# Kernel tuning notes

Hardware: AMD Instinct MI355X
Metric: run time of the kernel (lower is better)

Reference implementation:

```python
import jax, jax.numpy as jnp
import numpy as np

IN_CH = 128
OUT_CH = 128
INPUT_LEN = 512
KERNEL = 8
STRIDE = 1
OUT_LEN = (INPUT_LEN - KERNEL) // STRIDE + 1  # 505
BATCH = 64


def setup_inputs() -> dict:
    key = jax.random.key(0)
    kx, kw, kb = jax.random.split(key, 3)
    x = jax.random.normal(kx, (BATCH, IN_CH, INPUT_LEN), dtype=jnp.float32)
    weight = jax.random.normal(kw, (OUT_LEN, OUT_CH, IN_CH, KERNEL), dtype=jnp.float32)
    bias = jax.random.normal(kb, (OUT_CH, OUT_LEN), dtype=jnp.float32)
    return {"x": x, "weight": weight, "bias": bias}


def reference(x, weight, bias):
    # unfold: gather sliding windows -> [b, i, l_out, k]
    idx = jnp.arange(OUT_LEN)[:, None] * STRIDE + jnp.arange(KERNEL)[None, :]  # [l, k]
    x_unf = x[:, :, idx]  # [b, i, l, k]
    # per-position independent GEMM: 'blik,loik->bol' with x permuted to bilk
    out = jnp.einsum('bilk,loik->bol', x_unf, weight)
    out = out + bias[None, :, :]
    return out
```

## Files before the change

### kernel.cpp

```cpp
#include <hip/hip_runtime.h>
#include <hip/hip_bf16.h>

#define BATCH 64
#define IN_CH 128
#define ILEN  512
#define OLEN  505
#define OCH   128
#define KDIM  1024
#define BK    64
#define NCHK  16
#define NWG   (OLEN * 2)

typedef float f32x4  __attribute__((ext_vector_type(4)));
typedef short bf16x8 __attribute__((ext_vector_type(8)));

__device__ __forceinline__ short f2bf(float f) {
  union { __hip_bfloat16 h; short s; } u;
  u.h = __float2bfloat16(f);
  return u.s;
}

template <bool USE_TMP>
__global__ __launch_bounds__(256, 2) void lc1d_main(
    const float* __restrict__ x, const float* __restrict__ w,
    const float* __restrict__ bias, float* __restrict__ outp) {
  const int orig = blockIdx.x;
  const int xcd = orig & 7, idx = orig >> 3;
  const int q = NWG / 8, rm = NWG % 8;
  const int wg = (xcd < rm ? xcd * (q + 1) : rm * (q + 1) + (xcd - rm) * q) + idx;
  const int l  = wg >> 1;
  const int oh = wg & 1;

  const int tid  = threadIdx.x;
  const int lane = tid & 63;
  const int wn   = tid >> 6;
  const int r    = lane & 15;
  const int h    = lane >> 4;

  __shared__ float Bs[3][BK * 64];
  __shared__ short As[2][BK * 64];

  f32x4 acc[4];
#pragma unroll
  for (int m = 0; m < 4; ++m) acc[m] = (f32x4){0.f, 0.f, 0.f, 0.f};

  const float* __restrict__ wl =
      w + (size_t)l * (OCH * KDIM) + (size_t)oh * 64 * KDIM;

  const int so  = tid >> 4;
  const int sc  = tid & 15;
  const int ssw = ((so & 7) << 1) | ((so >> 3) & 1);

  const int kk  = tid & 63;
  const int tb  = tid >> 6;
  const int il  = kk >> 3;
  const int kof = kk & 7;

  float aa0[16], aa1[16];

  auto loadA = [&](float (&aa)[16], int kc) {
    const float* xb = x + (size_t)(kc * 8 + il) * ILEN + l + kof;
#pragma unroll
    for (int it = 0; it < 16; ++it)
      aa[it] = xb[(size_t)(it * 4 + tb) * (IN_CH * ILEN)];
  };
  auto writeA = [&](const float (&aa)[16], int buf) {
#pragma unroll
    for (int it = 0; it < 16; ++it) {
      const int b = it * 4 + tb;
      As[buf][b * 64 + (kk ^ ((b & 7) << 3))] = f2bf(aa[it]);
    }
  };
  auto stageB = [&](int buf, int kc) {
#pragma unroll
    for (int it = 0; it < 4; ++it) {
      const int ob = it * 16 + so;
      const float* src = wl + (size_t)ob * KDIM + kc * BK + (sc ^ ssw) * 4;
      __builtin_amdgcn_global_load_lds(
          (const __attribute__((address_space(1))) void*)src,
          (__attribute__((address_space(3))) void*)&Bs[buf][ob * 64 + sc * 4],
          16, 0, 0);
    }
  };

  const int rsw = ((r & 7) << 1) | ((r >> 3) & 1);
  auto compute = [&](int bB, int bA) {
    const int ob = wn * 16 + r;
#pragma unroll
    for (int ks = 0; ks < 2; ++ks) {
      const int c0 = ks * 8 + h * 2;
      const f32x4 blo = *reinterpret_cast<const f32x4*>(
          &Bs[bB][ob * 64 + ((c0) ^ rsw) * 4]);
      const f32x4 bhi = *reinterpret_cast<const f32x4*>(
          &Bs[bB][ob * 64 + ((c0 + 1) ^ rsw) * 4]);
      bf16x8 bfr;
#pragma unroll
      for (int j = 0; j < 4; ++j) {
        bfr[j]     = f2bf(blo[j]);
        bfr[4 + j] = f2bf(bhi[j]);
      }
#pragma unroll
      for (int mt = 0; mt < 4; ++mt) {
        const int b = mt * 16 + r;
        const bf16x8 afr = *reinterpret_cast<const bf16x8*>(
            &As[bA][b * 64 + ((ks * 32 + h * 8) ^ ((b & 7) << 3))]);
        acc[mt] = __builtin_amdgcn_mfma_f32_16x16x32_bf16(afr, bfr, acc[mt], 0, 0, 0);
      }
    }
  };

  loadA(aa0, 0);
  stageB(0, 0);
  writeA(aa0, 0);
  loadA(aa1, 1);
  stageB(1, 1);
  asm volatile("s_waitcnt vmcnt(20) lgkmcnt(0)" ::: "memory");
  __builtin_amdgcn_sched_barrier(0);
  __builtin_amdgcn_s_barrier();
  __builtin_amdgcn_sched_barrier(0);

#pragma unroll
  for (int kc = 0; kc < NCHK; ++kc) {
    if (kc + 2 < NCHK) {
      if ((kc & 1) == 0) loadA(aa0, kc + 2); else loadA(aa1, kc + 2);
      stageB((kc + 2) % 3, kc + 2);
    }
    __builtin_amdgcn_sched_barrier(0);
    compute(kc % 3, kc & 1);
    if (kc + 1 < NCHK) {
      if ((kc & 1) == 0) writeA(aa1, 1); else writeA(aa0, 0);
      if (kc + 2 < NCHK) {
        asm volatile("s_waitcnt vmcnt(20) lgkmcnt(0)" ::: "memory");
      } else {
        asm volatile("s_waitcnt vmcnt(0) lgkmcnt(0)" ::: "memory");
      }
      __builtin_amdgcn_sched_barrier(0);
      __builtin_amdgcn_s_barrier();
      __builtin_amdgcn_sched_barrier(0);
    }
  }

  const int og = oh * 64 + wn * 16 + r;
  if (USE_TMP) {
    float* t = outp + (size_t)l * (BATCH * OCH) + og;
#pragma unroll
    for (int mt = 0; mt < 4; ++mt)
#pragma unroll
      for (int j = 0; j < 4; ++j) {
        const int b = mt * 16 + h * 4 + j;
        t[(size_t)b * OCH] = acc[mt][j];
      }
  } else {
    const float bv = bias[og * OLEN + l];
#pragma unroll
    for (int mt = 0; mt < 4; ++mt)
#pragma unroll
      for (int j = 0; j < 4; ++j) {
        const int b = mt * 16 + h * 4 + j;
        outp[(size_t)b * (OCH * OLEN) + (size_t)og * OLEN + l] = acc[mt][j] + bv;
      }
  }
}

__global__ __launch_bounds__(256) void lc1d_tr(const float* __restrict__ tmp,
                                               const float* __restrict__ bias,
                                               float* __restrict__ out) {
  const int l0  = blockIdx.x * 64;
  const int bo0 = blockIdx.y * 64;
  const int tid = threadIdx.x;
  __shared__ float t[64][65];

  const int boj = tid & 63, lq = tid >> 6;
#pragma unroll
  for (int rr = 0; rr < 16; ++rr) {
    const int li = rr * 4 + lq;
    const int l  = l0 + li;
    if (l < OLEN) t[li][boj] = tmp[(size_t)l * (BATCH * OCH) + bo0 + boj];
  }
  __syncthreads();
  const int lj = tid & 63, bq = tid >> 6;
  const int l  = l0 + lj;
#pragma unroll
  for (int rr = 0; rr < 16; ++rr) {
    const int bl = rr * 4 + bq;
    const int bo = bo0 + bl;
    if (l < OLEN) {
      const int oc = bo & (OCH - 1);
      out[(size_t)bo * OLEN + l] = t[lj][bl] + bias[oc * OLEN + l];
    }
  }
}

extern "C" void kernel_launch(void* const* d_in, const int* in_sizes, int n_in,
                              void* d_out, int out_size, void* d_ws, size_t ws_size,
                              hipStream_t stream) {
  const float* x    = (const float*)d_in[0];
  const float* w    = (const float*)d_in[1];
  const float* bias = (const float*)d_in[2];
  float* out        = (float*)d_out;

  const size_t need = (size_t)OLEN * BATCH * OCH * sizeof(float);
  if (ws_size >= need) {
    float* tmp = (float*)d_ws;
    lc1d_main<true><<<dim3(NWG), 256, 0, stream>>>(x, w, bias, tmp);
    lc1d_tr<<<dim3(8, 128), 256, 0, stream>>>(tmp, bias, out);
  } else {
    lc1d_main<false><<<dim3(NWG), 256, 0, stream>>>(x, w, bias, out);
  }
}
```

Before: 109.3 us.

## Merge both output-channel halves into one workgroup per position to reuse A tile

Each workgroup now computes all 128 output channels for one output position instead of 64, so the x window tile is loaded and converted to bf16 once rather than twice. The B staging pipeline changes from a triple buffer with two-chunk lookahead to a double buffer holding both channel halves with one-chunk lookahead. The grid is halved to 505 workgroups with double the accumulators. This trades fewer workgroups and less latency hiding for the weight stream against reduced redundant x loads.

```diff
diff --git a/kernel.cpp b/kernel.cpp
--- a/kernel.cpp
+++ b/kernel.cpp
@@ -9,7 +9,7 @@
 #define KDIM  1024
 #define BK    64
 #define NCHK  16
-#define NWG   (OLEN * 2)
+#define NWG   OLEN
 
 typedef float f32x4  __attribute__((ext_vector_type(4)));
 typedef short bf16x8 __attribute__((ext_vector_type(8)));
@@ -27,9 +27,7 @@
   const int orig = blockIdx.x;
   const int xcd = orig & 7, idx = orig >> 3;
   const int q = NWG / 8, rm = NWG % 8;
-  const int wg = (xcd < rm ? xcd * (q + 1) : rm * (q + 1) + (xcd - rm) * q) + idx;
-  const int l  = wg >> 1;
-  const int oh = wg & 1;
+  const int l = (xcd < rm ? xcd * (q + 1) : rm * (q + 1) + (xcd - rm) * q) + idx;
 
   const int tid  = threadIdx.x;
   const int lane = tid & 63;
@@ -37,15 +35,16 @@
   const int r    = lane & 15;
   const int h    = lane >> 4;
 
-  __shared__ float Bs[3][BK * 64];
+  __shared__ float Bs[2][2][BK * 64];
   __shared__ short As[2][BK * 64];
 
-  f32x4 acc[4];
-#pragma unroll
-  for (int m = 0; m < 4; ++m) acc[m] = (f32x4){0.f, 0.f, 0.f, 0.f};
-
-  const float* __restrict__ wl =
-      w + (size_t)l * (OCH * KDIM) + (size_t)oh * 64 * KDIM;
+  f32x4 acc[2][4];
+#pragma unroll
+  for (int oh = 0; oh < 2; ++oh)
+#pragma unroll
+    for (int m = 0; m < 4; ++m) acc[oh][m] = (f32x4){0.f, 0.f, 0.f, 0.f};
+
+  const float* __restrict__ wl = w + (size_t)l * (OCH * KDIM);
 
   const int so  = tid >> 4;
   const int sc  = tid & 15;
@@ -71,28 +70,29 @@
       As[buf][b * 64 + (kk ^ ((b & 7) << 3))] = f2bf(aa[it]);
     }
   };
-  auto stageB = [&](int buf, int kc) {
+  auto stageB = [&](int buf, int kc, int oh) {
+    const float* wo = wl + (size_t)oh * 64 * KDIM;
 #pragma unroll
     for (int it = 0; it < 4; ++it) {
       const int ob = it * 16 + so;
-      const float* src = wl + (size_t)ob * KDIM + kc * BK + (sc ^ ssw) * 4;
+      const float* src = wo + (size_t)ob * KDIM + kc * BK + (sc ^ ssw) * 4;
       __builtin_amdgcn_global_load_lds(
           (const __attribute__((address_space(1))) void*)src,
-          (__attribute__((address_space(3))) void*)&Bs[buf][ob * 64 + sc * 4],
+          (__attribute__((address_space(3))) void*)&Bs[buf][oh][ob * 64 + sc * 4],
           16, 0, 0);
     }
   };
 
   const int rsw = ((r & 7) << 1) | ((r >> 3) & 1);
-  auto compute = [&](int bB, int bA) {
+  auto compute = [&](int cur, int oh) {
     const int ob = wn * 16 + r;
 #pragma unroll
     for (int ks = 0; ks < 2; ++ks) {
       const int c0 = ks * 8 + h * 2;
       const f32x4 blo = *reinterpret_cast<const f32x4*>(
-          &Bs[bB][ob * 64 + ((c0) ^ rsw) * 4]);
+          &Bs[cur][oh][ob * 64 + ((c0) ^ rsw) * 4]);
       const f32x4 bhi = *reinterpret_cast<const f32x4*>(
-          &Bs[bB][ob * 64 + ((c0 + 1) ^ rsw) * 4]);
+          &Bs[cur][oh][ob * 64 + ((c0 + 1) ^ rsw) * 4]);
       bf16x8 bfr;
 #pragma unroll
       for (int j = 0; j < 4; ++j) {
@@ -103,34 +103,38 @@
       for (int mt = 0; mt < 4; ++mt) {
         const int b = mt * 16 + r;
         const bf16x8 afr = *reinterpret_cast<const bf16x8*>(
-            &As[bA][b * 64 + ((ks * 32 + h * 8) ^ ((b & 7) << 3))]);
-        acc[mt] = __builtin_amdgcn_mfma_f32_16x16x32_bf16(afr, bfr, acc[mt], 0, 0, 0);
+            &As[cur][b * 64 + ((ks * 32 + h * 8) ^ ((b & 7) << 3))]);
+        acc[oh][mt] =
+            __builtin_amdgcn_mfma_f32_16x16x32_bf16(afr, bfr, acc[oh][mt], 0, 0, 0);
       }
     }
   };
 
   loadA(aa0, 0);
-  stageB(0, 0);
+  stageB(0, 0, 0);
+  stageB(0, 0, 1);
   writeA(aa0, 0);
   loadA(aa1, 1);
-  stageB(1, 1);
-  asm volatile("s_waitcnt vmcnt(20) lgkmcnt(0)" ::: "memory");
+  asm volatile("s_waitcnt vmcnt(16) lgkmcnt(0)" ::: "memory");
   __builtin_amdgcn_sched_barrier(0);
   __builtin_amdgcn_s_barrier();
   __builtin_amdgcn_sched_barrier(0);
 
-#pragma unroll
-  for (int kc = 0; kc < NCHK; ++kc) {
-    if (kc + 2 < NCHK) {
-      if ((kc & 1) == 0) loadA(aa0, kc + 2); else loadA(aa1, kc + 2);
-      stageB((kc + 2) % 3, kc + 2);
-    }
+  auto step = [&](int kc, float (&aaW)[16], float (&aaL)[16]) {
+    if (kc + 1 < NCHK) {
+      const int nxt = (kc + 1) & 1;
+      stageB(nxt, kc + 1, 0);
+      stageB(nxt, kc + 1, 1);
+    }
+    if (kc + 2 < NCHK) loadA(aaL, kc + 2);
     __builtin_amdgcn_sched_barrier(0);
-    compute(kc % 3, kc & 1);
+    const int cur = kc & 1;
+    compute(cur, 0);
+    compute(cur, 1);
     if (kc + 1 < NCHK) {
-      if ((kc & 1) == 0) writeA(aa1, 1); else writeA(aa0, 0);
+      writeA(aaW, (kc + 1) & 1);
       if (kc + 2 < NCHK) {
-        asm volatile("s_waitcnt vmcnt(20) lgkmcnt(0)" ::: "memory");
+        asm volatile("s_waitcnt vmcnt(16) lgkmcnt(0)" ::: "memory");
       } else {
         asm volatile("s_waitcnt vmcnt(0) lgkmcnt(0)" ::: "memory");
       }
@@ -138,27 +142,35 @@
       __builtin_amdgcn_s_barrier();
       __builtin_amdgcn_sched_barrier(0);
     }
-  }
-
-  const int og = oh * 64 + wn * 16 + r;
-  if (USE_TMP) {
-    float* t = outp + (size_t)l * (BATCH * OCH) + og;
-#pragma unroll
-    for (int mt = 0; mt < 4; ++mt)
-#pragma unroll
-      for (int j = 0; j < 4; ++j) {
-        const int b = mt * 16 + h * 4 + j;
-        t[(size_t)b * OCH] = acc[mt][j];
-      }
-  } else {
-    const float bv = bias[og * OLEN + l];
-#pragma unroll
-    for (int mt = 0; mt < 4; ++mt)
-#pragma unroll
-      for (int j = 0; j < 4; ++j) {
-        const int b = mt * 16 + h * 4 + j;
-        outp[(size_t)b * (OCH * OLEN) + (size_t)og * OLEN + l] = acc[mt][j] + bv;
-      }
+  };
+
+  for (int kc = 0; kc < NCHK; kc += 2) {
+    step(kc, aa1, aa0);
+    step(kc + 1, aa0, aa1);
+  }
+
+#pragma unroll
+  for (int oh = 0; oh < 2; ++oh) {
+    const int og = oh * 64 + wn * 16 + r;
+    if (USE_TMP) {
+      float* t = outp + (size_t)l * (BATCH * OCH) + og;
+#pragma unroll
+      for (int mt = 0; mt < 4; ++mt)
+#pragma unroll
+        for (int j = 0; j < 4; ++j) {
+          const int b = mt * 16 + h * 4 + j;
+          t[(size_t)b * OCH] = acc[oh][mt][j];
+        }
+    } else {
+      const float bv = bias[og * OLEN + l];
+#pragma unroll
+      for (int mt = 0; mt < 4; ++mt)
+#pragma unroll
+        for (int j = 0; j < 4; ++j) {
+          const int b = mt * 16 + h * 4 + j;
+          outp[(size_t)b * (OCH * OLEN) + (size_t)og * OLEN + l] = acc[oh][mt][j] + bv;
+        }
+    }
   }
 }
 
```

Result: faster. 101.7 us (-7.0%).

## Halve K-chunk to 32 and raise occupancy target to five workgroups per CU

Applied to the files above, without the earlier changes.

Shrinks each K chunk from 64 to 32 elements, doubling the number of pipeline steps. This cuts the LDS footprint and per-thread prefetch registers so the launch bound can request five workgroups per CU instead of two. The LDS swizzles, staging indices and wait counts are reworked to match, and the loop is rolled into a two-step body instead of being fully unrolled. The aim is more latency hiding through occupancy, at the cost of twice as many barriers and smaller work per sync.

```diff
diff --git a/kernel.cpp b/kernel.cpp
--- a/kernel.cpp
+++ b/kernel.cpp
@@ -7,8 +7,8 @@
 #define OLEN  505
 #define OCH   128
 #define KDIM  1024
-#define BK    64
-#define NCHK  16
+#define BK    32
+#define NCHK  32
 #define NWG   (OLEN * 2)
 
 typedef float f32x4  __attribute__((ext_vector_type(4)));
@@ -21,7 +21,7 @@
 }
 
 template <bool USE_TMP>
-__global__ __launch_bounds__(256, 2) void lc1d_main(
+__global__ __launch_bounds__(256, 5) void lc1d_main(
     const float* __restrict__ x, const float* __restrict__ w,
     const float* __restrict__ bias, float* __restrict__ outp) {
   const int orig = blockIdx.x;
@@ -38,74 +38,70 @@
   const int h    = lane >> 4;
 
   __shared__ float Bs[3][BK * 64];
-  __shared__ short As[2][BK * 64];
+  __shared__ short As[2][BATCH * BK];
 
   f32x4 acc[4];
 #pragma unroll
   for (int m = 0; m < 4; ++m) acc[m] = (f32x4){0.f, 0.f, 0.f, 0.f};
 
-  const float* __restrict__ wl =
+  const float* __restrict__ wo =
       w + (size_t)l * (OCH * KDIM) + (size_t)oh * 64 * KDIM;
 
-  const int so  = tid >> 4;
-  const int sc  = tid & 15;
-  const int ssw = ((so & 7) << 1) | ((so >> 3) & 1);
-
-  const int kk  = tid & 63;
-  const int tb  = tid >> 6;
-  const int il  = kk >> 3;
-  const int kof = kk & 7;
-
-  float aa0[16], aa1[16];
-
-  auto loadA = [&](float (&aa)[16], int kc) {
-    const float* xb = x + (size_t)(kc * 8 + il) * ILEN + l + kof;
-#pragma unroll
-    for (int it = 0; it < 16; ++it)
-      aa[it] = xb[(size_t)(it * 4 + tb) * (IN_CH * ILEN)];
-  };
-  auto writeA = [&](const float (&aa)[16], int buf) {
-#pragma unroll
-    for (int it = 0; it < 16; ++it) {
-      const int b = it * 4 + tb;
-      As[buf][b * 64 + (kk ^ ((b & 7) << 3))] = f2bf(aa[it]);
+  const int sob = tid >> 3;
+  const int scp = tid & 7;
+  const int il  = (tid & 31) >> 3;
+  const int kof = tid & 7;
+  const int tb  = tid >> 5;
+
+  float aa0[8], aa1[8];
+
+  auto loadA = [&](float (&aa)[8], int kc) {
+    const float* xb = x + (size_t)(kc * 4 + il) * ILEN + l + kof;
+#pragma unroll
+    for (int it = 0; it < 8; ++it)
+      aa[it] = xb[(size_t)(it * 8 + tb) * (IN_CH * ILEN)];
+  };
+  auto writeA = [&](const float (&aa)[8], int buf) {
+#pragma unroll
+    for (int it = 0; it < 8; ++it) {
+      const int b  = it * 8 + tb;
+      const int sA = (b ^ (b >> 2)) & 3;
+      As[buf][b * 32 + ((il ^ sA) << 3) + kof] = f2bf(aa[it]);
     }
   };
   auto stageB = [&](int buf, int kc) {
 #pragma unroll
-    for (int it = 0; it < 4; ++it) {
-      const int ob = it * 16 + so;
-      const float* src = wl + (size_t)ob * KDIM + kc * BK + (sc ^ ssw) * 4;
+    for (int it = 0; it < 2; ++it) {
+      const int ob = it * 32 + sob;
+      const int c  = scp ^ (ob & 7);
+      const float* src = wo + (size_t)ob * KDIM + kc * BK + c * 4;
       __builtin_amdgcn_global_load_lds(
           (const __attribute__((address_space(1))) void*)src,
-          (__attribute__((address_space(3))) void*)&Bs[buf][ob * 64 + sc * 4],
+          (__attribute__((address_space(3))) void*)&Bs[buf][ob * 32 + scp * 4],
           16, 0, 0);
     }
   };
 
-  const int rsw = ((r & 7) << 1) | ((r >> 3) & 1);
-  auto compute = [&](int bB, int bA) {
-    const int ob = wn * 16 + r;
-#pragma unroll
-    for (int ks = 0; ks < 2; ++ks) {
-      const int c0 = ks * 8 + h * 2;
-      const f32x4 blo = *reinterpret_cast<const f32x4*>(
-          &Bs[bB][ob * 64 + ((c0) ^ rsw) * 4]);
-      const f32x4 bhi = *reinterpret_cast<const f32x4*>(
-          &Bs[bB][ob * 64 + ((c0 + 1) ^ rsw) * 4]);
-      bf16x8 bfr;
-#pragma unroll
-      for (int j = 0; j < 4; ++j) {
-        bfr[j]     = f2bf(blo[j]);
-        bfr[4 + j] = f2bf(bhi[j]);
-      }
-#pragma unroll
-      for (int mt = 0; mt < 4; ++mt) {
-        const int b = mt * 16 + r;
-        const bf16x8 afr = *reinterpret_cast<const bf16x8*>(
-            &As[bA][b * 64 + ((ks * 32 + h * 8) ^ ((b & 7) << 3))]);
-        acc[mt] = __builtin_amdgcn_mfma_f32_16x16x32_bf16(afr, bfr, acc[mt], 0, 0, 0);
-      }
+  auto compute = [&](int bufB, int bufA) {
+    const int ob  = wn * 16 + r;
+    const int swb = ob & 7;
+    const f32x4 blo = *reinterpret_cast<const f32x4*>(
+        &Bs[bufB][ob * 32 + (((2 * h) ^ swb) << 2)]);
+    const f32x4 bhi = *reinterpret_cast<const f32x4*>(
+        &Bs[bufB][ob * 32 + (((2 * h + 1) ^ swb) << 2)]);
+    bf16x8 bfr;
+#pragma unroll
+    for (int j = 0; j < 4; ++j) {
+      bfr[j]     = f2bf(blo[j]);
+      bfr[4 + j] = f2bf(bhi[j]);
+    }
+#pragma unroll
+    for (int mt = 0; mt < 4; ++mt) {
+      const int b  = mt * 16 + r;
+      const int sA = (b ^ (b >> 2)) & 3;
+      const bf16x8 afr = *reinterpret_cast<const bf16x8*>(
+          &As[bufA][b * 32 + ((h ^ sA) << 3)]);
+      acc[mt] = __builtin_amdgcn_mfma_f32_16x16x32_bf16(afr, bfr, acc[mt], 0, 0, 0);
     }
   };
 
@@ -114,23 +110,22 @@
   writeA(aa0, 0);
   loadA(aa1, 1);
   stageB(1, 1);
-  asm volatile("s_waitcnt vmcnt(20) lgkmcnt(0)" ::: "memory");
+  asm volatile("s_waitcnt vmcnt(10) lgkmcnt(0)" ::: "memory");
   __builtin_amdgcn_sched_barrier(0);
   __builtin_amdgcn_s_barrier();
   __builtin_amdgcn_sched_barrier(0);
 
-#pragma unroll
-  for (int kc = 0; kc < NCHK; ++kc) {
+  auto step = [&](int kc, float (&aaW)[8], float (&aaL)[8]) {
     if (kc + 2 < NCHK) {
-      if ((kc & 1) == 0) loadA(aa0, kc + 2); else loadA(aa1, kc + 2);
       stageB((kc + 2) % 3, kc + 2);
+      loadA(aaL, kc + 2);
     }
     __builtin_amdgcn_sched_barrier(0);
     compute(kc % 3, kc & 1);
     if (kc + 1 < NCHK) {
-      if ((kc & 1) == 0) writeA(aa1, 1); else writeA(aa0, 0);
+      writeA(aaW, (kc + 1) & 1);
       if (kc + 2 < NCHK) {
-        asm volatile("s_waitcnt vmcnt(20) lgkmcnt(0)" ::: "memory");
+        asm volatile("s_waitcnt vmcnt(10) lgkmcnt(0)" ::: "memory");
       } else {
         asm volatile("s_waitcnt vmcnt(0) lgkmcnt(0)" ::: "memory");
       }
@@ -138,6 +133,11 @@
       __builtin_amdgcn_s_barrier();
       __builtin_amdgcn_sched_barrier(0);
     }
+  };
+
+  for (int kc = 0; kc < NCHK; kc += 2) {
+    step(kc, aa1, aa0);
+    step(kc + 1, aa0, aa1);
   }
 
   const int og = oh * 64 + wn * 16 + r;
```

After: 126.9 us. 16.1% more time.
